# Kernel optimization log

Hardware: AMD Instinct MI355X
Metric: run time of the kernel (lower is better)

## Reference

```python
import jax, jax.numpy as jnp
import numpy as np

B, D = 500000, 3
EPS = 1e-8

def _matrix_sqrt_H(A):
    # Hermitian sqrt via eigh: Q diag((L^2)^0.25) Q^T  (matches torch code incl. |L| handling)
    L, Q = jnp.linalg.eigh(A)
    return jnp.einsum('bij,bj,bkj->bik', Q, (L ** 2) ** 0.25, Q)

def setup_inputs() -> dict:
    key = jax.random.key(0)
    k1, k2, k3, k4 = jax.random.split(key, 4)
    miu_1 = jax.random.normal(k1, (B, D), dtype=jnp.float32)
    miu_2 = jax.random.normal(k2, (B, D), dtype=jnp.float32)
    eye = jnp.eye(D, dtype=jnp.float32)
    M1 = jax.random.normal(k3, (B, D, D), dtype=jnp.float32)
    M2 = jax.random.normal(k4, (B, D, D), dtype=jnp.float32)
    # SPD covariances, as produced by a Gaussian-splatting pipeline
    cov_1 = 0.1 * jnp.einsum('bij,bkj->bik', M1, M1) + 1e-3 * eye
    cov_2 = 0.1 * jnp.einsum('bij,bkj->bik', M2, M2) + 1e-3 * eye
    return {"miu_1": miu_1, "miu_2": miu_2, "cov_1": cov_1, "cov_2": cov_2}

def reference(miu_1, miu_2, cov_1, cov_2):
    eye = jnp.eye(cov_1.shape[-1], dtype=cov_1.dtype)
    A_sqrt = _matrix_sqrt_H(cov_1 + eye * EPS)
    A_sqrt_inv = jnp.linalg.inv(A_sqrt + eye * EPS)
    C = jnp.einsum('bij,bjk,blk->bil', A_sqrt, cov_2, A_sqrt)  # A_sqrt cov_2 A_sqrt^T
    C_sqrt = _matrix_sqrt_H(C + eye * EPS)
    cov_velocity = jnp.einsum('bij,bjk,blk->bil', A_sqrt, C_sqrt, A_sqrt_inv)
    cov_velocity = cov_velocity + jnp.swapaxes(cov_velocity, -1, -2) - 2.0 * cov_1
    return (miu_2 - miu_1, cov_velocity)
```

## Files before the change

kernel.cpp:

```cpp
#include <hip/hip_runtime.h>
#include <math.h>

#define EPS 1e-8f

__device__ __forceinline__ void jrot(float A[3][3], float Q[3][3], int p, int q, int r) {
    float apq  = A[p][q];
    float diff = A[q][q] - A[p][p];
    float theta = diff * __builtin_amdgcn_rcpf(2.0f * apq);
    float t = __builtin_amdgcn_rcpf(fabsf(theta) + sqrtf(fmaf(theta, theta, 1.0f)));
    t = copysignf(t, theta);
    t = (fabsf(apq) < 1e-30f) ? 0.0f : t;
    float c = __builtin_amdgcn_rsqf(fmaf(t, t, 1.0f));
    float s = t * c;
    float tapq = t * apq;
    A[p][p] -= tapq;
    A[q][q] += tapq;
    A[p][q] = 0.0f; A[q][p] = 0.0f;
    float arp = A[r][p], arq = A[r][q];
    A[r][p] = fmaf(c, arp, -s * arq); A[p][r] = A[r][p];
    A[r][q] = fmaf(c, arq,  s * arp); A[q][r] = A[r][q];
    #pragma unroll
    for (int i = 0; i < 3; ++i) {
        float qip = Q[i][p], qiq = Q[i][q];
        Q[i][p] = fmaf(c, qip, -s * qiq);
        Q[i][q] = fmaf(s, qip,  c * qiq);
    }
}

__device__ __forceinline__ void eigh3f(float A[3][3], float Q[3][3]) {
    Q[0][0] = 1.0f; Q[0][1] = 0.0f; Q[0][2] = 0.0f;
    Q[1][0] = 0.0f; Q[1][1] = 1.0f; Q[1][2] = 0.0f;
    Q[2][0] = 0.0f; Q[2][1] = 0.0f; Q[2][2] = 1.0f;
    #pragma unroll
    for (int sweep = 0; sweep < 5; ++sweep) {
        jrot(A, Q, 0, 1, 2);
        jrot(A, Q, 0, 2, 1);
        jrot(A, Q, 1, 2, 0);
    }
}

__global__ __launch_bounds__(256) void wasserstein_log_kernel(
    const float* __restrict__ miu1, const float* __restrict__ miu2,
    const float* __restrict__ cov1, const float* __restrict__ cov2,
    float* __restrict__ out, int B)
{
    int b = blockIdx.x * blockDim.x + threadIdx.x;
    if (b >= B) return;

    out[3*b + 0] = miu2[3*b + 0] - miu1[3*b + 0];
    out[3*b + 1] = miu2[3*b + 1] - miu1[3*b + 1];
    out[3*b + 2] = miu2[3*b + 2] - miu1[3*b + 2];

    float c1[3][3], c2m[3][3];
    #pragma unroll
    for (int i = 0; i < 3; ++i)
        #pragma unroll
        for (int j = 0; j < 3; ++j) {
            c1[i][j]  = cov1[9*b + 3*i + j];
            c2m[i][j] = cov2[9*b + 3*i + j];
        }

    float A[3][3];
    #pragma unroll
    for (int i = 0; i < 3; ++i)
        #pragma unroll
        for (int j = 0; j < 3; ++j)
            A[i][j] = c1[i][j] + (i == j ? EPS : 0.0f);
    float Q[3][3];
    eigh3f(A, Q);

    float s[3], si[3];
    #pragma unroll
    for (int k = 0; k < 3; ++k) {
        s[k]  = sqrtf(fabsf(A[k][k]));
        si[k] = __builtin_amdgcn_rcpf(s[k] + EPS);
    }

    float S[3][3], Sinv[3][3];
    #pragma unroll
    for (int i = 0; i < 3; ++i)
        #pragma unroll
        for (int j = 0; j < 3; ++j) {
            S[i][j]    = fmaf(Q[i][0]*s[0],  Q[j][0], fmaf(Q[i][1]*s[1],  Q[j][1], Q[i][2]*s[2]  * Q[j][2]));
            Sinv[i][j] = fmaf(Q[i][0]*si[0], Q[j][0], fmaf(Q[i][1]*si[1], Q[j][1], Q[i][2]*si[2] * Q[j][2]));
        }

    float T[3][3];
    #pragma unroll
    for (int i = 0; i < 3; ++i)
        #pragma unroll
        for (int k = 0; k < 3; ++k)
            T[i][k] = fmaf(S[i][0], c2m[0][k], fmaf(S[i][1], c2m[1][k], S[i][2]*c2m[2][k]));
    float C[3][3];
    #pragma unroll
    for (int i = 0; i < 3; ++i)
        #pragma unroll
        for (int l = 0; l < 3; ++l)
            C[i][l] = fmaf(T[i][0], S[l][0], fmaf(T[i][1], S[l][1], T[i][2]*S[l][2]))
                      + (i == l ? EPS : 0.0f);

    float Qc[3][3];
    eigh3f(C, Qc);
    float t0 = sqrtf(fabsf(C[0][0])), t1 = sqrtf(fabsf(C[1][1])), t2 = sqrtf(fabsf(C[2][2]));
    float Csq[3][3];
    #pragma unroll
    for (int i = 0; i < 3; ++i)
        #pragma unroll
        for (int j = 0; j < 3; ++j)
            Csq[i][j] = fmaf(Qc[i][0]*t0, Qc[j][0], fmaf(Qc[i][1]*t1, Qc[j][1], Qc[i][2]*t2 * Qc[j][2]));

    float T2[3][3];
    #pragma unroll
    for (int i = 0; i < 3; ++i)
        #pragma unroll
        for (int k = 0; k < 3; ++k)
            T2[i][k] = fmaf(S[i][0], Csq[0][k], fmaf(S[i][1], Csq[1][k], S[i][2]*Csq[2][k]));
    float V[3][3];
    #pragma unroll
    for (int i = 0; i < 3; ++i)
        #pragma unroll
        for (int l = 0; l < 3; ++l)
            V[i][l] = fmaf(T2[i][0], Sinv[l][0], fmaf(T2[i][1], Sinv[l][1], T2[i][2]*Sinv[l][2]));

    float* out_cov = out + (size_t)3 * B;
    #pragma unroll
    for (int i = 0; i < 3; ++i)
        #pragma unroll
        for (int j = 0; j < 3; ++j)
            out_cov[9*b + 3*i + j] = V[i][j] + V[j][i] - 2.0f*c1[i][j];
}

extern "C" void kernel_launch(void* const* d_in, const int* in_sizes, int n_in,
                              void* d_out, int out_size, void* d_ws, size_t ws_size,
                              hipStream_t stream) {
    const float* miu1 = (const float*)d_in[0];
    const float* miu2 = (const float*)d_in[1];
    const float* cov1 = (const float*)d_in[2];
    const float* cov2 = (const float*)d_in[3];
    float* out = (float*)d_out;
    int B = in_sizes[0] / 3;
    int threads = 256;
    int blocks = (B + threads - 1) / threads;
    hipLaunchKernelGGL(wasserstein_log_kernel, dim3(blocks), dim3(threads), 0, stream,
                       miu1, miu2, cov1, cov2, out, B);
}
```

Measured before the change: 108.4 us.

## Rewrite 3x3 Wasserstein log with symmetric-only Jacobi and eigenbasis algebra

Replaces the generic 5-sweep Jacobi eigensolver with a cheaper rotation formula (rsqrt-based, no division) and three sweeps, the first specialised to skip identity multiplies. The C matrix is now formed in the eigenbasis of cov_1 (Q^T cov2 Q scaled by sqrt eigenvalues), so the explicit S and Sinv matrices are never built, and only the symmetric upper triangle is loaded and computed. Occupancy is also hinted via launch bounds. It reduces ALU work per thread, at the risk of lower accuracy from fewer sweeps and from the reformulated inverse.

```diff
diff --git a/kernel.cpp b/kernel.cpp
--- a/kernel.cpp
+++ b/kernel.cpp
@@ -3,43 +3,68 @@
 
 #define EPS 1e-8f
 
-__device__ __forceinline__ void jrot(float A[3][3], float Q[3][3], int p, int q, int r) {
-    float apq  = A[p][q];
-    float diff = A[q][q] - A[p][p];
-    float theta = diff * __builtin_amdgcn_rcpf(2.0f * apq);
-    float t = __builtin_amdgcn_rcpf(fabsf(theta) + sqrtf(fmaf(theta, theta, 1.0f)));
-    t = copysignf(t, theta);
-    t = (fabsf(apq) < 1e-30f) ? 0.0f : t;
-    float c = __builtin_amdgcn_rsqf(fmaf(t, t, 1.0f));
-    float s = t * c;
-    float tapq = t * apq;
-    A[p][p] -= tapq;
-    A[q][q] += tapq;
-    A[p][q] = 0.0f; A[q][p] = 0.0f;
-    float arp = A[r][p], arq = A[r][q];
-    A[r][p] = fmaf(c, arp, -s * arq); A[p][r] = A[r][p];
-    A[r][q] = fmaf(c, arq,  s * arp); A[q][r] = A[r][q];
+__device__ __forceinline__ void jangle(float app, float aqq, float apq,
+                                       float &c, float &s, float &app2, float &aqq2) {
+    float h     = aqq - app;
+    float ah    = fabsf(h) + 1e-18f;
+    float v     = apq + apq;
+    float rad   = fmaf(ah, ah, v * v);
+    float rr    = __builtin_amdgcn_rsqf(rad);
+    float c2h   = fmaf(0.5f * ah, rr, 0.5f);
+    float rc2   = __builtin_amdgcn_rsqf(c2h);
+    c = c2h * rc2;
+    float apq_s = (h < 0.0f) ? -apq : apq;
+    s = apq_s * (rr * rc2);
+    float dl    = copysignf(0.5f * (rad * rr - ah), h);
+    app2 = app - dl;
+    aqq2 = aqq + dl;
+}
+
+__device__ __forceinline__ void eigh3(
+    float &a00, float &a01, float &a02, float &a11, float &a12, float &a22,
+    float &q00, float &q01, float &q02,
+    float &q10, float &q11, float &q12,
+    float &q20, float &q21, float &q22)
+{
+    float c, s, x, y, t0, t1;
+    jangle(a00, a11, a01, c, s, x, y); a00 = x; a11 = y; a01 = 0.0f;
+    t0 = a02; t1 = a12; a02 = fmaf(c, t0, -s * t1); a12 = fmaf(c, t1, s * t0);
+    q00 = c; q01 = s; q10 = -s; q11 = c;
+
+    jangle(a00, a22, a02, c, s, x, y); a00 = x; a22 = y; a02 = 0.0f;
+    t0 = a01; t1 = a12; a01 = fmaf(c, t0, -s * t1); a12 = fmaf(c, t1, s * t0);
+    q02 = s * q00; q12 = s * q10; q20 = -s; q22 = c;
+    q00 = c * q00; q10 = c * q10;
+
+    jangle(a11, a22, a12, c, s, x, y); a11 = x; a22 = y; a12 = 0.0f;
+    t0 = a01; t1 = a02; a01 = fmaf(c, t0, -s * t1); a02 = fmaf(c, t1, s * t0);
+    t0 = q01; t1 = q02; q01 = fmaf(c, t0, -s * t1); q02 = fmaf(s, t0, c * t1);
+    t0 = q11; t1 = q12; q11 = fmaf(c, t0, -s * t1); q12 = fmaf(s, t0, c * t1);
+    q21 = -s * q22; q22 = c * q22;
+
     #pragma unroll
-    for (int i = 0; i < 3; ++i) {
-        float qip = Q[i][p], qiq = Q[i][q];
-        Q[i][p] = fmaf(c, qip, -s * qiq);
-        Q[i][q] = fmaf(s, qip,  c * qiq);
+    for (int sw = 0; sw < 2; ++sw) {
+        jangle(a00, a11, a01, c, s, x, y); a00 = x; a11 = y; a01 = 0.0f;
+        t0 = a02; t1 = a12; a02 = fmaf(c, t0, -s * t1); a12 = fmaf(c, t1, s * t0);
+        t0 = q00; t1 = q01; q00 = fmaf(c, t0, -s * t1); q01 = fmaf(s, t0, c * t1);
+        t0 = q10; t1 = q11; q10 = fmaf(c, t0, -s * t1); q11 = fmaf(s, t0, c * t1);
+        t0 = q20; t1 = q21; q20 = fmaf(c, t0, -s * t1); q21 = fmaf(s, t0, c * t1);
+
+        jangle(a00, a22, a02, c, s, x, y); a00 = x; a22 = y; a02 = 0.0f;
+        t0 = a01; t1 = a12; a01 = fmaf(c, t0, -s * t1); a12 = fmaf(c, t1, s * t0);
+        t0 = q00; t1 = q02; q00 = fmaf(c, t0, -s * t1); q02 = fmaf(s, t0, c * t1);
+        t0 = q10; t1 = q12; q10 = fmaf(c, t0, -s * t1); q12 = fmaf(s, t0, c * t1);
+        t0 = q20; t1 = q22; q20 = fmaf(c, t0, -s * t1); q22 = fmaf(s, t0, c * t1);
+
+        jangle(a11, a22, a12, c, s, x, y); a11 = x; a22 = y; a12 = 0.0f;
+        t0 = a01; t1 = a02; a01 = fmaf(c, t0, -s * t1); a02 = fmaf(c, t1, s * t0);
+        t0 = q01; t1 = q02; q01 = fmaf(c, t0, -s * t1); q02 = fmaf(s, t0, c * t1);
+        t0 = q11; t1 = q12; q11 = fmaf(c, t0, -s * t1); q12 = fmaf(s, t0, c * t1);
+        t0 = q21; t1 = q22; q21 = fmaf(c, t0, -s * t1); q22 = fmaf(s, t0, c * t1);
     }
 }
 
-__device__ __forceinline__ void eigh3f(float A[3][3], float Q[3][3]) {
-    Q[0][0] = 1.0f; Q[0][1] = 0.0f; Q[0][2] = 0.0f;
-    Q[1][0] = 0.0f; Q[1][1] = 1.0f; Q[1][2] = 0.0f;
-    Q[2][0] = 0.0f; Q[2][1] = 0.0f; Q[2][2] = 1.0f;
-    #pragma unroll
-    for (int sweep = 0; sweep < 5; ++sweep) {
-        jrot(A, Q, 0, 1, 2);
-        jrot(A, Q, 0, 2, 1);
-        jrot(A, Q, 1, 2, 0);
-    }
-}
-
-__global__ __launch_bounds__(256) void wasserstein_log_kernel(
+__global__ __launch_bounds__(256, 7) void wasserstein_log_kernel(
     const float* __restrict__ miu1, const float* __restrict__ miu2,
     const float* __restrict__ cov1, const float* __restrict__ cov2,
     float* __restrict__ out, int B)
@@ -51,83 +76,112 @@
     out[3*b + 1] = miu2[3*b + 1] - miu1[3*b + 1];
     out[3*b + 2] = miu2[3*b + 2] - miu1[3*b + 2];
 
-    float c1[3][3], c2m[3][3];
-    #pragma unroll
-    for (int i = 0; i < 3; ++i)
-        #pragma unroll
-        for (int j = 0; j < 3; ++j) {
-            c1[i][j]  = cov1[9*b + 3*i + j];
-            c2m[i][j] = cov2[9*b + 3*i + j];
-        }
-
-    float A[3][3];
-    #pragma unroll
-    for (int i = 0; i < 3; ++i)
-        #pragma unroll
-        for (int j = 0; j < 3; ++j)
-            A[i][j] = c1[i][j] + (i == j ? EPS : 0.0f);
-    float Q[3][3];
-    eigh3f(A, Q);
-
-    float s[3], si[3];
-    #pragma unroll
-    for (int k = 0; k < 3; ++k) {
-        s[k]  = sqrtf(fabsf(A[k][k]));
-        si[k] = __builtin_amdgcn_rcpf(s[k] + EPS);
-    }
-
-    float S[3][3], Sinv[3][3];
-    #pragma unroll
-    for (int i = 0; i < 3; ++i)
-        #pragma unroll
-        for (int j = 0; j < 3; ++j) {
-            S[i][j]    = fmaf(Q[i][0]*s[0],  Q[j][0], fmaf(Q[i][1]*s[1],  Q[j][1], Q[i][2]*s[2]  * Q[j][2]));
-            Sinv[i][j] = fmaf(Q[i][0]*si[0], Q[j][0], fmaf(Q[i][1]*si[1], Q[j][1], Q[i][2]*si[2] * Q[j][2]));
-        }
-
-    float T[3][3];
-    #pragma unroll
-    for (int i = 0; i < 3; ++i)
-        #pragma unroll
-        for (int k = 0; k < 3; ++k)
-            T[i][k] = fmaf(S[i][0], c2m[0][k], fmaf(S[i][1], c2m[1][k], S[i][2]*c2m[2][k]));
-    float C[3][3];
-    #pragma unroll
-    for (int i = 0; i < 3; ++i)
-        #pragma unroll
-        for (int l = 0; l < 3; ++l)
-            C[i][l] = fmaf(T[i][0], S[l][0], fmaf(T[i][1], S[l][1], T[i][2]*S[l][2]))
-                      + (i == l ? EPS : 0.0f);
-
-    float Qc[3][3];
-    eigh3f(C, Qc);
-    float t0 = sqrtf(fabsf(C[0][0])), t1 = sqrtf(fabsf(C[1][1])), t2 = sqrtf(fabsf(C[2][2]));
-    float Csq[3][3];
-    #pragma unroll
-    for (int i = 0; i < 3; ++i)
-        #pragma unroll
-        for (int j = 0; j < 3; ++j)
-            Csq[i][j] = fmaf(Qc[i][0]*t0, Qc[j][0], fmaf(Qc[i][1]*t1, Qc[j][1], Qc[i][2]*t2 * Qc[j][2]));
-
-    float T2[3][3];
-    #pragma unroll
-    for (int i = 0; i < 3; ++i)
-        #pragma unroll
-        for (int k = 0; k < 3; ++k)
-            T2[i][k] = fmaf(S[i][0], Csq[0][k], fmaf(S[i][1], Csq[1][k], S[i][2]*Csq[2][k]));
-    float V[3][3];
-    #pragma unroll
-    for (int i = 0; i < 3; ++i)
-        #pragma unroll
-        for (int l = 0; l < 3; ++l)
-            V[i][l] = fmaf(T2[i][0], Sinv[l][0], fmaf(T2[i][1], Sinv[l][1], T2[i][2]*Sinv[l][2]));
-
-    float* out_cov = out + (size_t)3 * B;
-    #pragma unroll
-    for (int i = 0; i < 3; ++i)
-        #pragma unroll
-        for (int j = 0; j < 3; ++j)
-            out_cov[9*b + 3*i + j] = V[i][j] + V[j][i] - 2.0f*c1[i][j];
+    const float* c1p = cov1 + 9*(size_t)b;
+    const float* c2p = cov2 + 9*(size_t)b;
+    float k00 = c1p[0], k01 = c1p[1], k02 = c1p[2],
+          k11 = c1p[4], k12 = c1p[5], k22 = c1p[8];
+    float m00 = c2p[0], m01 = c2p[1], m02 = c2p[2],
+          m11 = c2p[4], m12 = c2p[5], m22 = c2p[8];
+
+    float a00 = k00 + EPS, a01 = k01, a02 = k02,
+          a11 = k11 + EPS, a12 = k12, a22 = k22 + EPS;
+    float q00, q01, q02, q10, q11, q12, q20, q21, q22;
+    eigh3(a00, a01, a02, a11, a12, a22,
+          q00, q01, q02, q10, q11, q12, q20, q21, q22);
+
+    float w0 = fmaxf(fabsf(a00), 1e-12f);
+    float w1 = fmaxf(fabsf(a11), 1e-12f);
+    float w2 = fmaxf(fabsf(a22), 1e-12f);
+    float di0 = __builtin_amdgcn_rsqf(w0), di1 = __builtin_amdgcn_rsqf(w1),
+          di2 = __builtin_amdgcn_rsqf(w2);
+    float d0 = w0 * di0, d1 = w1 * di1, d2 = w2 * di2;
+
+    float T00 = fmaf(m00, q00, fmaf(m01, q10, m02 * q20));
+    float T01 = fmaf(m00, q01, fmaf(m01, q11, m02 * q21));
+    float T02 = fmaf(m00, q02, fmaf(m01, q12, m02 * q22));
+    float T10 = fmaf(m01, q00, fmaf(m11, q10, m12 * q20));
+    float T11 = fmaf(m01, q01, fmaf(m11, q11, m12 * q21));
+    float T12 = fmaf(m01, q02, fmaf(m11, q12, m12 * q22));
+    float T20 = fmaf(m02, q00, fmaf(m12, q10, m22 * q20));
+    float T21 = fmaf(m02, q01, fmaf(m12, q11, m22 * q21));
+    float T22 = fmaf(m02, q02, fmaf(m12, q12, m22 * q22));
+
+    float g00 = fmaf(q00, T00, fmaf(q10, T10, q20 * T20));
+    float g01 = fmaf(q00, T01, fmaf(q10, T11, q20 * T21));
+    float g02 = fmaf(q00, T02, fmaf(q10, T12, q20 * T22));
+    float g11 = fmaf(q01, T01, fmaf(q11, T11, q21 * T21));
+    float g12 = fmaf(q01, T02, fmaf(q11, T12, q21 * T22));
+    float g22 = fmaf(q02, T02, fmaf(q12, T12, q22 * T22));
+
+    float cp00 = fmaf(w0, g00, EPS);
+    float cp11 = fmaf(w1, g11, EPS);
+    float cp22 = fmaf(w2, g22, EPS);
+    float cp01 = d0 * d1 * g01;
+    float cp02 = d0 * d2 * g02;
+    float cp12 = d1 * d2 * g12;
+
+    float e00, e01, e02, e10, e11, e12, e20, e21, e22;
+    eigh3(cp00, cp01, cp02, cp11, cp12, cp22,
+          e00, e01, e02, e10, e11, e12, e20, e21, e22);
+    float u0 = fmaxf(fabsf(cp00), 1e-12f);
+    float u1 = fmaxf(fabsf(cp11), 1e-12f);
+    float u2 = fmaxf(fabsf(cp22), 1e-12f);
+    float ts0 = u0 * __builtin_amdgcn_rsqf(u0);
+    float ts1 = u1 * __builtin_amdgcn_rsqf(u1);
+    float ts2 = u2 * __builtin_amdgcn_rsqf(u2);
+
+    float Ed00 = d0*e00, Ed01 = d0*e01, Ed02 = d0*e02;
+    float Ed10 = d1*e10, Ed11 = d1*e11, Ed12 = d1*e12;
+    float Ed20 = d2*e20, Ed21 = d2*e21, Ed22 = d2*e22;
+    float Ei00 = di0*e00, Ei01 = di0*e01, Ei02 = di0*e02;
+    float Ei10 = di1*e10, Ei11 = di1*e11, Ei12 = di1*e12;
+    float Ei20 = di2*e20, Ei21 = di2*e21, Ei22 = di2*e22;
+
+    float U00 = fmaf(q00, Ed00, fmaf(q01, Ed10, q02 * Ed20));
+    float U01 = fmaf(q00, Ed01, fmaf(q01, Ed11, q02 * Ed21));
+    float U02 = fmaf(q00, Ed02, fmaf(q01, Ed12, q02 * Ed22));
+    float U10 = fmaf(q10, Ed00, fmaf(q11, Ed10, q12 * Ed20));
+    float U11 = fmaf(q10, Ed01, fmaf(q11, Ed11, q12 * Ed21));
+    float U12 = fmaf(q10, Ed02, fmaf(q11, Ed12, q12 * Ed22));
+    float U20 = fmaf(q20, Ed00, fmaf(q21, Ed10, q22 * Ed20));
+    float U21 = fmaf(q20, Ed01, fmaf(q21, Ed11, q22 * Ed21));
+    float U22 = fmaf(q20, Ed02, fmaf(q21, Ed12, q22 * Ed22));
+
+    float P00 = fmaf(q00, Ei00, fmaf(q01, Ei10, q02 * Ei20));
+    float P01 = fmaf(q00, Ei01, fmaf(q01, Ei11, q02 * Ei21));
+    float P02 = fmaf(q00, Ei02, fmaf(q01, Ei12, q02 * Ei22));
+    float P10 = fmaf(q10, Ei00, fmaf(q11, Ei10, q12 * Ei20));
+    float P11 = fmaf(q10, Ei01, fmaf(q11, Ei11, q12 * Ei21));
+    float P12 = fmaf(q10, Ei02, fmaf(q11, Ei12, q12 * Ei22));
+    float P20 = fmaf(q20, Ei00, fmaf(q21, Ei10, q22 * Ei20));
+    float P21 = fmaf(q20, Ei01, fmaf(q21, Ei11, q22 * Ei21));
+    float P22 = fmaf(q20, Ei02, fmaf(q21, Ei12, q22 * Ei22));
+
+    float A0 = ts0 * U00, A1 = ts1 * U01, A2 = ts2 * U02;
+    float B0 = ts0 * U10, B1 = ts1 * U11, B2 = ts2 * U12;
+    float C0 = ts0 * U20, C1 = ts1 * U21, C2 = ts2 * U22;
+
+    float W00 = 2.0f * fmaf(A0, P00, fmaf(A1, P01, A2 * P02));
+    float W11 = 2.0f * fmaf(B0, P10, fmaf(B1, P11, B2 * P12));
+    float W22 = 2.0f * fmaf(C0, P20, fmaf(C1, P21, C2 * P22));
+    float W01 = fmaf(A0, P10, fmaf(A1, P11, fmaf(A2, P12,
+                fmaf(B0, P00, fmaf(B1, P01, B2 * P02)))));
+    float W02 = fmaf(A0, P20, fmaf(A1, P21, fmaf(A2, P22,
+                fmaf(C0, P00, fmaf(C1, P01, C2 * P02)))));
+    float W12 = fmaf(B0, P20, fmaf(B1, P21, fmaf(B2, P22,
+                fmaf(C0, P10, fmaf(C1, P11, C2 * P12)))));
+
+    float o00 = fmaf(-2.0f, k00, W00);
+    float o01 = fmaf(-2.0f, k01, W01);
+    float o02 = fmaf(-2.0f, k02, W02);
+    float o11 = fmaf(-2.0f, k11, W11);
+    float o12 = fmaf(-2.0f, k12, W12);
+    float o22 = fmaf(-2.0f, k22, W22);
+
+    float* oc = out + (size_t)3 * B + 9*(size_t)b;
+    oc[0] = o00; oc[1] = o01; oc[2] = o02;
+    oc[3] = o01; oc[4] = o11; oc[5] = o12;
+    oc[6] = o02; oc[7] = o12; oc[8] = o22;
 }
 
 extern "C" void kernel_launch(void* const* d_in, const int* in_sizes, int n_in,
```

New measurement: 97.61 us. -10.0%, faster.
